# Kernel optimization log

Measured on AMD Instinct MI355X. Metric: run time of the kernel, lower is better.

Reference implementation:

```python
import jax, jax.numpy as jnp
import numpy as np

B = 8192
MAX_ATOMS = 768
EPS = 1e-7


def setup_inputs() -> dict:
    key = jax.random.key(0)
    k1, k2, k3 = jax.random.split(key, 3)
    inp = jax.random.normal(k1, (B, 3 * MAX_ATOMS), dtype=jnp.float32)
    tgt = jax.random.normal(k2, (B, 3 * MAX_ATOMS), dtype=jnp.float32)
    # variable atom counts; keep >= MAX_ATOMS//2 so centering/division is well-posed
    num_atoms = jax.random.randint(k3, (B,), MAX_ATOMS // 2, MAX_ATOMS + 1, dtype=jnp.int64)
    return {"input": inp, "target": tgt, "num_atoms": num_atoms}


def _kabsch_rmsd(inp, tgt, num_atoms):
    b = inp.shape[0]
    m = inp.shape[1] // 3
    X = inp.reshape(b, m, 3)
    Y = tgt.reshape(b, m, 3)
    mask = (jnp.arange(m)[None, :] < num_atoms[:, None])[..., None]  # [B, M, 1]
    n = num_atoms.astype(inp.dtype)[:, None]  # [B, 1]
    # center over the valid atoms of each sample
    Xc = (X - (jnp.where(mask, X, 0).sum(axis=1) / n)[:, None, :])
    Yc = (Y - (jnp.where(mask, Y, 0).sum(axis=1) / n)[:, None, :])
    Xc = jnp.where(mask, Xc, 0)
    Yc = jnp.where(mask, Yc, 0)
    # 3x3 correlation matrix per sample (Kabsch)
    R = jnp.einsum('bai,baj->bij', Xc, Yc)  # [B, 3, 3]
    s = jnp.linalg.svd(R, compute_uv=False)  # [B, 3], descending
    d = jnp.sign(jnp.linalg.det(R))  # proper-rotation correction
    trace = s[:, 0] + s[:, 1] + d * s[:, 2]
    e = jnp.sum(Xc * Xc, axis=(1, 2)) + jnp.sum(Yc * Yc, axis=(1, 2)) - 2.0 * trace
    n1 = num_atoms.astype(inp.dtype)
    return jnp.sqrt(jnp.maximum(e, 0.0) / n1 + EPS)


def reference(input, target, num_atoms):
    return _kabsch_rmsd(input, target, num_atoms)
```

## Files before the change

### kernel.cpp

```cpp
#include <hip/hip_runtime.h>
#include <math.h>

#ifndef M_PI
#define M_PI 3.14159265358979323846
#endif

#define MA 768

__device__ __forceinline__ float dpp_red_add(float v) {
    v += __int_as_float(__builtin_amdgcn_update_dpp(0, __float_as_int(v), 0x111, 0xf, 0xf, true));
    v += __int_as_float(__builtin_amdgcn_update_dpp(0, __float_as_int(v), 0x112, 0xf, 0xf, true));
    v += __int_as_float(__builtin_amdgcn_update_dpp(0, __float_as_int(v), 0x114, 0xf, 0xe, true));
    v += __int_as_float(__builtin_amdgcn_update_dpp(0, __float_as_int(v), 0x118, 0xf, 0xc, true));
    v += __int_as_float(__builtin_amdgcn_update_dpp(0, __float_as_int(v), 0x142, 0xa, 0xf, true));
    v += __int_as_float(__builtin_amdgcn_update_dpp(0, __float_as_int(v), 0x143, 0xc, 0xf, true));
    return v;
}

__global__ __launch_bounds__(256, 4) void kabsch_kernel(
    const float* __restrict__ inp, const float* __restrict__ tgt,
    const int* __restrict__ natoms, float* __restrict__ out)
{
    const int wave = threadIdx.x >> 6;
    const int lane = threadIdx.x & 63;
    const int b = blockIdx.x * 4 + wave;
    const int n = natoms[b];
    const float* __restrict__ X = inp + (size_t)b * (3 * MA);
    const float* __restrict__ Y = tgt + (size_t)b * (3 * MA);

    const int a0 = 12 * lane;

    const float4 f4z = make_float4(0.f, 0.f, 0.f, 0.f);
    float4 vx[9], vy[9];
#pragma unroll
    for (int k = 0; k < 9; ++k) { vx[k] = f4z; vy[k] = f4z; }

    if (a0 < n) {
        const float4* px = (const float4*)(X + 3 * a0);
        const float4* py = (const float4*)(Y + 3 * a0);
#pragma unroll
        for (int k = 0; k < 9; ++k) vx[k] = px[k];
#pragma unroll
        for (int k = 0; k < 9; ++k) vy[k] = py[k];
    }
    __builtin_amdgcn_sched_barrier(0);

    float ax[36], ay[36];
#pragma unroll
    for (int k = 0; k < 9; ++k) {
        *(float4*)&ax[4 * k] = vx[k];
        *(float4*)&ay[4 * k] = vy[k];
    }

    float sx0 = 0.f, sx1 = 0.f, sx2 = 0.f;
    float sy0 = 0.f, sy1 = 0.f, sy2 = 0.f;
    float c00 = 0.f, c01 = 0.f, c02 = 0.f;
    float c10 = 0.f, c11 = 0.f, c12 = 0.f;
    float c20 = 0.f, c21 = 0.f, c22 = 0.f;
    float nx2 = 0.f, ny2 = 0.f;

#pragma unroll
    for (int j = 0; j < 12; ++j) {
        const bool v = (a0 + j) < n;
        const float x0 = v ? ax[3 * j + 0] : 0.f;
        const float x1 = v ? ax[3 * j + 1] : 0.f;
        const float x2 = v ? ax[3 * j + 2] : 0.f;
        const float y0 = v ? ay[3 * j + 0] : 0.f;
        const float y1 = v ? ay[3 * j + 1] : 0.f;
        const float y2 = v ? ay[3 * j + 2] : 0.f;
        sx0 += x0; sx1 += x1; sx2 += x2;
        sy0 += y0; sy1 += y1; sy2 += y2;
        c00 = fmaf(x0, y0, c00); c01 = fmaf(x0, y1, c01); c02 = fmaf(x0, y2, c02);
        c10 = fmaf(x1, y0, c10); c11 = fmaf(x1, y1, c11); c12 = fmaf(x1, y2, c12);
        c20 = fmaf(x2, y0, c20); c21 = fmaf(x2, y1, c21); c22 = fmaf(x2, y2, c22);
        nx2 = fmaf(x0, x0, nx2); nx2 = fmaf(x1, x1, nx2); nx2 = fmaf(x2, x2, nx2);
        ny2 = fmaf(y0, y0, ny2); ny2 = fmaf(y1, y1, ny2); ny2 = fmaf(y2, y2, ny2);
    }

    sx0 = dpp_red_add(sx0); sx1 = dpp_red_add(sx1); sx2 = dpp_red_add(sx2);
    sy0 = dpp_red_add(sy0); sy1 = dpp_red_add(sy1); sy2 = dpp_red_add(sy2);
    c00 = dpp_red_add(c00); c01 = dpp_red_add(c01); c02 = dpp_red_add(c02);
    c10 = dpp_red_add(c10); c11 = dpp_red_add(c11); c12 = dpp_red_add(c12);
    c20 = dpp_red_add(c20); c21 = dpp_red_add(c21); c22 = dpp_red_add(c22);
    nx2 = dpp_red_add(nx2); ny2 = dpp_red_add(ny2);

    if (lane == 63) {
        const float inv_n = 1.0f / (float)n;

        const float R00 = fmaf(-sx0 * inv_n, sy0, c00);
        const float R01 = fmaf(-sx0 * inv_n, sy1, c01);
        const float R02 = fmaf(-sx0 * inv_n, sy2, c02);
        const float R10 = fmaf(-sx1 * inv_n, sy0, c10);
        const float R11 = fmaf(-sx1 * inv_n, sy1, c11);
        const float R12 = fmaf(-sx1 * inv_n, sy2, c12);
        const float R20 = fmaf(-sx2 * inv_n, sy0, c20);
        const float R21 = fmaf(-sx2 * inv_n, sy1, c21);
        const float R22 = fmaf(-sx2 * inv_n, sy2, c22);
        const float ex = nx2 - (sx0 * sx0 + sx1 * sx1 + sx2 * sx2) * inv_n;
        const float ey = ny2 - (sy0 * sy0 + sy1 * sy1 + sy2 * sy2) * inv_n;

        const float A00 = R00 * R00 + R10 * R10 + R20 * R20;
        const float A11 = R01 * R01 + R11 * R11 + R21 * R21;
        const float A22 = R02 * R02 + R12 * R12 + R22 * R22;
        const float A01 = R00 * R01 + R10 * R11 + R20 * R21;
        const float A02 = R00 * R02 + R10 * R12 + R20 * R22;
        const float A12 = R01 * R02 + R11 * R12 + R21 * R22;

        const float detR = R00 * (R11 * R22 - R12 * R21)
                         - R01 * (R10 * R22 - R12 * R20)
                         + R02 * (R10 * R21 - R11 * R20);

        const float q = (A00 + A11 + A22) * (1.0f / 3.0f);
        const float p1 = A01 * A01 + A02 * A02 + A12 * A12;
        const float b00 = A00 - q, b11 = A11 - q, b22 = A22 - q;
        const float p2 = b00 * b00 + b11 * b11 + b22 * b22 + 2.0f * p1;
        float e0, e1, e2;
        if (p2 <= 0.0f) {
            e0 = e1 = e2 = q;
        } else {
            const float p = sqrtf(p2 * (1.0f / 6.0f));
            const float ip = 1.0f / p;
            const float B00 = b00 * ip, B11 = b11 * ip, B22 = b22 * ip;
            const float B01 = A01 * ip, B02 = A02 * ip, B12 = A12 * ip;
            const float detB = B00 * (B11 * B22 - B12 * B12)
                             - B01 * (B01 * B22 - B12 * B02)
                             + B02 * (B01 * B12 - B11 * B02);
            float rr = 0.5f * detB;
            rr = fminf(1.0f, fmaxf(-1.0f, rr));
            const float phi = acosf(rr) * (1.0f / 3.0f);
            const float cA = __cosf(phi);
            const float cC = __cosf(phi + (float)(2.0 * M_PI / 3.0));
            e0 = fmaf(2.0f * p, cA, q);
            e2 = fmaf(2.0f * p, cC, q);
            e1 = 3.0f * q - e0 - e2;
        }
        const float s0 = sqrtf(fmaxf(e0, 0.0f));
        const float s1 = sqrtf(fmaxf(e1, 0.0f));
        const float s2 = sqrtf(fmaxf(e2, 0.0f));
        const float d = (detR > 0.0f) ? 1.0f : ((detR < 0.0f) ? -1.0f : 0.0f);
        const float tr = s0 + s1 + d * s2;
        const float e = ex + ey - 2.0f * tr;
        out[b] = sqrtf(fmaxf(e, 0.0f) * inv_n + 1e-7f);
    }
}

extern "C" void kernel_launch(void* const* d_in, const int* in_sizes, int n_in,
                              void* d_out, int out_size, void* d_ws, size_t ws_size,
                              hipStream_t stream) {
    const float* inp = (const float*)d_in[0];
    const float* tgt = (const float*)d_in[1];
    const int* natoms = (const int*)d_in[2];
    float* out = (float*)d_out;
    (void)d_ws; (void)ws_size; (void)n_in; (void)in_sizes;
    kabsch_kernel<<<dim3(out_size / 4), dim3(256), 0, stream>>>(inp, tgt, natoms, out);
}
```

Baseline: 24.42 us.

## Split each sample across two waves with uneven atom ranges and LDS combine

Each sample is now handled by a two-wave block. Wave 0 covers atoms 0-511 with 8 atoms per lane, and wave 1 covers atoms 512-767 with 4 atoms per lane. Wave 1 writes its reduced partial sums to shared memory and wave 0 combines them before the 3x3 eigenvalue step. This doubles the number of waves per sample, aiming for more memory parallelism and less per-lane register load. The cost is a block barrier, LDS traffic, and unbalanced work between the two waves, and wave 1 is often idle when the atom count is below 512.

```diff
diff --git a/kernel.cpp b/kernel.cpp
--- a/kernel.cpp
+++ b/kernel.cpp
@@ -17,50 +17,21 @@
     return v;
 }
 
-__global__ __launch_bounds__(256, 4) void kabsch_kernel(
-    const float* __restrict__ inp, const float* __restrict__ tgt,
-    const int* __restrict__ natoms, float* __restrict__ out)
-{
-    const int wave = threadIdx.x >> 6;
-    const int lane = threadIdx.x & 63;
-    const int b = blockIdx.x * 4 + wave;
-    const int n = natoms[b];
-    const float* __restrict__ X = inp + (size_t)b * (3 * MA);
-    const float* __restrict__ Y = tgt + (size_t)b * (3 * MA);
-
-    const int a0 = 12 * lane;
-
-    const float4 f4z = make_float4(0.f, 0.f, 0.f, 0.f);
-    float4 vx[9], vy[9];
-#pragma unroll
-    for (int k = 0; k < 9; ++k) { vx[k] = f4z; vy[k] = f4z; }
-
-    if (a0 < n) {
-        const float4* px = (const float4*)(X + 3 * a0);
-        const float4* py = (const float4*)(Y + 3 * a0);
-#pragma unroll
-        for (int k = 0; k < 9; ++k) vx[k] = px[k];
-#pragma unroll
-        for (int k = 0; k < 9; ++k) vy[k] = py[k];
-    }
-    __builtin_amdgcn_sched_barrier(0);
-
-    float ax[36], ay[36];
-#pragma unroll
-    for (int k = 0; k < 9; ++k) {
-        *(float4*)&ax[4 * k] = vx[k];
-        *(float4*)&ay[4 * k] = vy[k];
-    }
-
+struct Sums {
     float sx0 = 0.f, sx1 = 0.f, sx2 = 0.f;
     float sy0 = 0.f, sy1 = 0.f, sy2 = 0.f;
     float c00 = 0.f, c01 = 0.f, c02 = 0.f;
     float c10 = 0.f, c11 = 0.f, c12 = 0.f;
     float c20 = 0.f, c21 = 0.f, c22 = 0.f;
     float nx2 = 0.f, ny2 = 0.f;
-
-#pragma unroll
-    for (int j = 0; j < 12; ++j) {
+};
+
+template<int NA>
+__device__ __forceinline__ void accum(const float* ax, const float* ay,
+                                      int a0, int n, Sums& S)
+{
+#pragma unroll
+    for (int j = 0; j < NA; ++j) {
         const bool v = (a0 + j) < n;
         const float x0 = v ? ax[3 * j + 0] : 0.f;
         const float x1 = v ? ax[3 * j + 1] : 0.f;
@@ -68,23 +39,104 @@
         const float y0 = v ? ay[3 * j + 0] : 0.f;
         const float y1 = v ? ay[3 * j + 1] : 0.f;
         const float y2 = v ? ay[3 * j + 2] : 0.f;
-        sx0 += x0; sx1 += x1; sx2 += x2;
-        sy0 += y0; sy1 += y1; sy2 += y2;
-        c00 = fmaf(x0, y0, c00); c01 = fmaf(x0, y1, c01); c02 = fmaf(x0, y2, c02);
-        c10 = fmaf(x1, y0, c10); c11 = fmaf(x1, y1, c11); c12 = fmaf(x1, y2, c12);
-        c20 = fmaf(x2, y0, c20); c21 = fmaf(x2, y1, c21); c22 = fmaf(x2, y2, c22);
-        nx2 = fmaf(x0, x0, nx2); nx2 = fmaf(x1, x1, nx2); nx2 = fmaf(x2, x2, nx2);
-        ny2 = fmaf(y0, y0, ny2); ny2 = fmaf(y1, y1, ny2); ny2 = fmaf(y2, y2, ny2);
-    }
-
-    sx0 = dpp_red_add(sx0); sx1 = dpp_red_add(sx1); sx2 = dpp_red_add(sx2);
-    sy0 = dpp_red_add(sy0); sy1 = dpp_red_add(sy1); sy2 = dpp_red_add(sy2);
-    c00 = dpp_red_add(c00); c01 = dpp_red_add(c01); c02 = dpp_red_add(c02);
-    c10 = dpp_red_add(c10); c11 = dpp_red_add(c11); c12 = dpp_red_add(c12);
-    c20 = dpp_red_add(c20); c21 = dpp_red_add(c21); c22 = dpp_red_add(c22);
-    nx2 = dpp_red_add(nx2); ny2 = dpp_red_add(ny2);
-
-    if (lane == 63) {
+        S.sx0 += x0; S.sx1 += x1; S.sx2 += x2;
+        S.sy0 += y0; S.sy1 += y1; S.sy2 += y2;
+        S.c00 = fmaf(x0, y0, S.c00); S.c01 = fmaf(x0, y1, S.c01); S.c02 = fmaf(x0, y2, S.c02);
+        S.c10 = fmaf(x1, y0, S.c10); S.c11 = fmaf(x1, y1, S.c11); S.c12 = fmaf(x1, y2, S.c12);
+        S.c20 = fmaf(x2, y0, S.c20); S.c21 = fmaf(x2, y1, S.c21); S.c22 = fmaf(x2, y2, S.c22);
+        S.nx2 = fmaf(x0, x0, S.nx2); S.nx2 = fmaf(x1, x1, S.nx2); S.nx2 = fmaf(x2, x2, S.nx2);
+        S.ny2 = fmaf(y0, y0, S.ny2); S.ny2 = fmaf(y1, y1, S.ny2); S.ny2 = fmaf(y2, y2, S.ny2);
+    }
+}
+
+__global__ __launch_bounds__(128, 4) void kabsch_kernel(
+    const float* __restrict__ inp, const float* __restrict__ tgt,
+    const int* __restrict__ natoms, float* __restrict__ out)
+{
+    const int wave = threadIdx.x >> 6;
+    const int lane = threadIdx.x & 63;
+    const int b = blockIdx.x;
+    const int n = natoms[b];
+    const float* __restrict__ X = inp + (size_t)b * (3 * MA);
+    const float* __restrict__ Y = tgt + (size_t)b * (3 * MA);
+
+    __shared__ float part[17];
+
+    Sums S;
+
+    if (wave == 0) {
+        const int a0 = 8 * lane;
+        float4 vx[6], vy[6];
+        const float4 f4z = make_float4(0.f, 0.f, 0.f, 0.f);
+#pragma unroll
+        for (int k = 0; k < 6; ++k) { vx[k] = f4z; vy[k] = f4z; }
+        if (a0 < n) {
+            const float4* px = (const float4*)(X + 24 * lane);
+            const float4* py = (const float4*)(Y + 24 * lane);
+#pragma unroll
+            for (int k = 0; k < 6; ++k) vx[k] = px[k];
+#pragma unroll
+            for (int k = 0; k < 6; ++k) vy[k] = py[k];
+        }
+        __builtin_amdgcn_sched_barrier(0);
+
+        float ax[24], ay[24];
+#pragma unroll
+        for (int k = 0; k < 6; ++k) {
+            *(float4*)&ax[4 * k] = vx[k];
+            *(float4*)&ay[4 * k] = vy[k];
+        }
+        accum<8>(ax, ay, a0, n, S);
+    } else {
+        const int a1 = 512 + 4 * lane;
+        float4 vx[3], vy[3];
+        const float4 f4z = make_float4(0.f, 0.f, 0.f, 0.f);
+#pragma unroll
+        for (int k = 0; k < 3; ++k) { vx[k] = f4z; vy[k] = f4z; }
+        if (a1 < n) {
+            const float4* px = (const float4*)(X + 1536 + 12 * lane);
+            const float4* py = (const float4*)(Y + 1536 + 12 * lane);
+#pragma unroll
+            for (int k = 0; k < 3; ++k) vx[k] = px[k];
+#pragma unroll
+            for (int k = 0; k < 3; ++k) vy[k] = py[k];
+        }
+        __builtin_amdgcn_sched_barrier(0);
+
+        float ax[12], ay[12];
+#pragma unroll
+        for (int k = 0; k < 3; ++k) {
+            *(float4*)&ax[4 * k] = vx[k];
+            *(float4*)&ay[4 * k] = vy[k];
+        }
+        accum<4>(ax, ay, a1, n, S);
+    }
+
+    S.sx0 = dpp_red_add(S.sx0); S.sx1 = dpp_red_add(S.sx1); S.sx2 = dpp_red_add(S.sx2);
+    S.sy0 = dpp_red_add(S.sy0); S.sy1 = dpp_red_add(S.sy1); S.sy2 = dpp_red_add(S.sy2);
+    S.c00 = dpp_red_add(S.c00); S.c01 = dpp_red_add(S.c01); S.c02 = dpp_red_add(S.c02);
+    S.c10 = dpp_red_add(S.c10); S.c11 = dpp_red_add(S.c11); S.c12 = dpp_red_add(S.c12);
+    S.c20 = dpp_red_add(S.c20); S.c21 = dpp_red_add(S.c21); S.c22 = dpp_red_add(S.c22);
+    S.nx2 = dpp_red_add(S.nx2); S.ny2 = dpp_red_add(S.ny2);
+
+    if (wave == 1 && lane == 63) {
+        part[ 0] = S.sx0; part[ 1] = S.sx1; part[ 2] = S.sx2;
+        part[ 3] = S.sy0; part[ 4] = S.sy1; part[ 5] = S.sy2;
+        part[ 6] = S.c00; part[ 7] = S.c01; part[ 8] = S.c02;
+        part[ 9] = S.c10; part[10] = S.c11; part[11] = S.c12;
+        part[12] = S.c20; part[13] = S.c21; part[14] = S.c22;
+        part[15] = S.nx2; part[16] = S.ny2;
+    }
+    __syncthreads();
+
+    if (wave == 0 && lane == 63) {
+        const float sx0 = S.sx0 + part[ 0], sx1 = S.sx1 + part[ 1], sx2 = S.sx2 + part[ 2];
+        const float sy0 = S.sy0 + part[ 3], sy1 = S.sy1 + part[ 4], sy2 = S.sy2 + part[ 5];
+        const float c00 = S.c00 + part[ 6], c01 = S.c01 + part[ 7], c02 = S.c02 + part[ 8];
+        const float c10 = S.c10 + part[ 9], c11 = S.c11 + part[10], c12 = S.c12 + part[11];
+        const float c20 = S.c20 + part[12], c21 = S.c21 + part[13], c22 = S.c22 + part[14];
+        const float nx2 = S.nx2 + part[15], ny2 = S.ny2 + part[16];
+
         const float inv_n = 1.0f / (float)n;
 
         const float R00 = fmaf(-sx0 * inv_n, sy0, c00);
@@ -152,5 +204,5 @@
     const int* natoms = (const int*)d_in[2];
     float* out = (float*)d_out;
     (void)d_ws; (void)ws_size; (void)n_in; (void)in_sizes;
-    kabsch_kernel<<<dim3(out_size / 4), dim3(256), 0, stream>>>(inp, tgt, natoms, out);
-}
+    kabsch_kernel<<<dim3(out_size), dim3(128), 0, stream>>>(inp, tgt, natoms, out);
+}
```

Result: slower. 25.49 us (+4.4%).

## Process four samples per wave with double-buffered register prefetch

Applied to the files above, without the earlier changes.

Each wave now handles four consecutive samples instead of one. The next sample's rows are loaded into a second register buffer while the current one is reduced, with scheduling barriers keeping the loads issued before the compute. The grid shrinks fourfold and launch bounds drop to two blocks per CU to make room for the extra registers. The aim is to hide load latency within a wave, at the cost of fewer waves in flight across the GPU for a kernel that is already near bandwidth-bound.

```diff
diff --git a/kernel.cpp b/kernel.cpp
--- a/kernel.cpp
+++ b/kernel.cpp
@@ -6,6 +6,7 @@
 #endif
 
 #define MA 768
+#define ROWF (3 * MA)
 
 __device__ __forceinline__ float dpp_red_add(float v) {
     v += __int_as_float(__builtin_amdgcn_update_dpp(0, __float_as_int(v), 0x111, 0xf, 0xf, true));
@@ -17,24 +18,12 @@
     return v;
 }
 
-__global__ __launch_bounds__(256, 4) void kabsch_kernel(
-    const float* __restrict__ inp, const float* __restrict__ tgt,
-    const int* __restrict__ natoms, float* __restrict__ out)
+__device__ __forceinline__ void load_rows(const float* __restrict__ X,
+                                          const float* __restrict__ Y,
+                                          int lane, int n,
+                                          float4 (&vx)[9], float4 (&vy)[9])
 {
-    const int wave = threadIdx.x >> 6;
-    const int lane = threadIdx.x & 63;
-    const int b = blockIdx.x * 4 + wave;
-    const int n = natoms[b];
-    const float* __restrict__ X = inp + (size_t)b * (3 * MA);
-    const float* __restrict__ Y = tgt + (size_t)b * (3 * MA);
-
     const int a0 = 12 * lane;
-
-    const float4 f4z = make_float4(0.f, 0.f, 0.f, 0.f);
-    float4 vx[9], vy[9];
-#pragma unroll
-    for (int k = 0; k < 9; ++k) { vx[k] = f4z; vy[k] = f4z; }
-
     if (a0 < n) {
         const float4* px = (const float4*)(X + 3 * a0);
         const float4* py = (const float4*)(Y + 3 * a0);
@@ -43,8 +32,13 @@
 #pragma unroll
         for (int k = 0; k < 9; ++k) vy[k] = py[k];
     }
-    __builtin_amdgcn_sched_barrier(0);
+}
 
+__device__ __forceinline__ void process(const float4 (&vx)[9],
+                                        const float4 (&vy)[9],
+                                        int lane, int n, int b,
+                                        float* __restrict__ out)
+{
     float ax[36], ay[36];
 #pragma unroll
     for (int k = 0; k < 9; ++k) {
@@ -59,6 +53,7 @@
     float c20 = 0.f, c21 = 0.f, c22 = 0.f;
     float nx2 = 0.f, ny2 = 0.f;
 
+    const int a0 = 12 * lane;
 #pragma unroll
     for (int j = 0; j < 12; ++j) {
         const bool v = (a0 + j) < n;
@@ -144,6 +139,43 @@
     }
 }
 
+__global__ __launch_bounds__(256, 2) void kabsch_kernel(
+    const float* __restrict__ inp, const float* __restrict__ tgt,
+    const int* __restrict__ natoms, float* __restrict__ out)
+{
+    const int wave = threadIdx.x >> 6;
+    const int lane = threadIdx.x & 63;
+    const int w = blockIdx.x * 4 + wave;
+    const int b0 = w * 4;
+
+    const int n0 = natoms[b0 + 0];
+    const int n1 = natoms[b0 + 1];
+    const int n2 = natoms[b0 + 2];
+    const int n3 = natoms[b0 + 3];
+
+    const float* __restrict__ X0 = inp + (size_t)b0 * ROWF;
+    const float* __restrict__ Y0 = tgt + (size_t)b0 * ROWF;
+
+    float4 Axv[9], Ayv[9], Bxv[9], Byv[9];
+
+    load_rows(X0, Y0, lane, n0, Axv, Ayv);
+    __builtin_amdgcn_sched_barrier(0);
+
+    load_rows(X0 + ROWF, Y0 + ROWF, lane, n1, Bxv, Byv);
+    __builtin_amdgcn_sched_barrier(0);
+    process(Axv, Ayv, lane, n0, b0 + 0, out);
+
+    load_rows(X0 + 2 * ROWF, Y0 + 2 * ROWF, lane, n2, Axv, Ayv);
+    __builtin_amdgcn_sched_barrier(0);
+    process(Bxv, Byv, lane, n1, b0 + 1, out);
+
+    load_rows(X0 + 3 * ROWF, Y0 + 3 * ROWF, lane, n3, Bxv, Byv);
+    __builtin_amdgcn_sched_barrier(0);
+    process(Axv, Ayv, lane, n2, b0 + 2, out);
+
+    process(Bxv, Byv, lane, n3, b0 + 3, out);
+}
+
 extern "C" void kernel_launch(void* const* d_in, const int* in_sizes, int n_in,
                               void* d_out, int out_size, void* d_ws, size_t ws_size,
                               hipStream_t stream) {
@@ -152,5 +184,5 @@
     const int* natoms = (const int*)d_in[2];
     float* out = (float*)d_out;
     (void)d_ws; (void)ws_size; (void)n_in; (void)in_sizes;
-    kabsch_kernel<<<dim3(out_size / 4), dim3(256), 0, stream>>>(inp, tgt, natoms, out);
+    kabsch_kernel<<<dim3(out_size / 16), dim3(256), 0, stream>>>(inp, tgt, natoms, out);
 }
```

After: 28.96 us. 18.6% more time.
